# Performance work log

Hardware: AMD Instinct MI355X
Metric: run time of the kernel (lower is better)

Reference implementation:

```python
import jax, jax.numpy as jnp
import numpy as np

EMB = 256
HID = 512
VOCAB = 32000
SRC_LEN = 50
TRG_LEN = 50
BATCH = 64


def lstm_layer(x, h0, c0, Wih, Whh, b):
    """x: [T,B,in]; h0,c0: [B,H]; Wih: [4H,in]; Whh: [4H,H]; b: [4H].
    PyTorch gate order i,f,g,o. Returns (ys [T,B,H], hT, cT)."""
    def step(carry, xt):
        h, c = carry
        g = xt @ Wih.T + h @ Whh.T + b
        i, f, gg, o = jnp.split(g, 4, axis=-1)
        c = jax.nn.sigmoid(f) * c + jax.nn.sigmoid(i) * jnp.tanh(gg)
        h = jax.nn.sigmoid(o) * jnp.tanh(c)
        return (h, c), h
    (hT, cT), ys = jax.lax.scan(step, (h0, c0), x)
    return ys, hT, cT


def setup_inputs() -> dict:
    key = jax.random.key(0)
    ks = jax.random.split(key, 20)
    s = 0.05
    d = {
        'src': jax.random.randint(ks[0], (SRC_LEN, BATCH), 0, VOCAB),
        'trg': jax.random.randint(ks[1], (TRG_LEN, BATCH), 0, VOCAB),
        'enc_emb': jax.random.normal(ks[2], (VOCAB, EMB), jnp.float32) * s,
        'enc_Wih0': jax.random.normal(ks[3], (4 * HID, EMB), jnp.float32) * s,
        'enc_Whh0': jax.random.normal(ks[4], (4 * HID, HID), jnp.float32) * s,
        'enc_b0': jnp.zeros((4 * HID,), jnp.float32),
        'enc_Wih1': jax.random.normal(ks[5], (4 * HID, HID), jnp.float32) * s,
        'enc_Whh1': jax.random.normal(ks[6], (4 * HID, HID), jnp.float32) * s,
        'enc_b1': jnp.zeros((4 * HID,), jnp.float32),
        'dec_emb': jax.random.normal(ks[7], (VOCAB, EMB), jnp.float32) * s,
        'dec_Wih0': jax.random.normal(ks[8], (4 * HID, EMB), jnp.float32) * s,
        'dec_Whh0': jax.random.normal(ks[9], (4 * HID, HID), jnp.float32) * s,
        'dec_b0': jnp.zeros((4 * HID,), jnp.float32),
        'dec_Wih1': jax.random.normal(ks[10], (4 * HID, HID), jnp.float32) * s,
        'dec_Whh1': jax.random.normal(ks[11], (4 * HID, HID), jnp.float32) * s,
        'dec_b1': jnp.zeros((4 * HID,), jnp.float32),
        'out_W': jax.random.normal(ks[12], (VOCAB, HID), jnp.float32) * s,
        'out_b': jnp.zeros((VOCAB,), jnp.float32),
    }
    return d


def reference(src, trg, enc_emb, enc_Wih0, enc_Whh0, enc_b0, enc_Wih1, enc_Whh1,
              enc_b1, dec_emb, dec_Wih0, dec_Whh0, dec_b0, dec_Wih1, dec_Whh1,
              dec_b1, out_W, out_b):
    B = src.shape[1]
    z = jnp.zeros((B, HID), enc_emb.dtype)
    # Encoder: 2-layer LSTM over src, keep final (h, c) per layer
    xe = enc_emb[src]                                   # [S,B,E]
    y0, h0, c0 = lstm_layer(xe, z, z, enc_Wih0, enc_Whh0, enc_b0)
    _, h1, c1 = lstm_layer(y0, z, z, enc_Wih1, enc_Whh1, enc_b1)
    # Decoder with teacher forcing: inputs are trg[0:T-1]
    xd = dec_emb[trg[:-1]]                              # [T-1,B,E]
    d0, _, _ = lstm_layer(xd, h0, c0, dec_Wih0, dec_Whh0, dec_b0)
    d1, _, _ = lstm_layer(d0, h1, c1, dec_Wih1, dec_Whh1, dec_b1)
    preds = d1 @ out_W.T + out_b                        # [T-1,B,V]
    return preds
```

## Files before the change

kernel.cpp:

```cpp
#include <hip/hip_runtime.h>
#include <hip/hip_bf16.h>

#define BATCH 64
#define HID 512
#define EMB 256
#define VOCAB 32000
#define G4 2048

typedef __attribute__((ext_vector_type(8))) short short8;
typedef __attribute__((ext_vector_type(4))) float f32x4;
typedef __attribute__((ext_vector_type(4))) unsigned short ush4;

__global__ __launch_bounds__(256) void zero_kernel(float* p, int n){
    int i = blockIdx.x*256 + threadIdx.x;
    if (i < n) p[i] = 0.f;
}

__device__ __forceinline__ unsigned short bf16_rne(float x){
    unsigned b = __float_as_uint(x);
    return (unsigned short)((b + 0x7fffu + ((b >> 16) & 1u)) >> 16);
}
__device__ __forceinline__ void split2(float x, unsigned short& h, unsigned short& l){
    h = bf16_rne(x);
    l = bf16_rne(x - __uint_as_float((unsigned)h << 16));
}

__global__ __launch_bounds__(256) void embed_kernel(const int* __restrict__ tok,
                                                    const float* __restrict__ emb,
                                                    float* __restrict__ out, int T){
    int i = blockIdx.x*256 + threadIdx.x;
    int n = T*BATCH*(EMB/4);
    if (i >= n) return;
    int e4 = i % (EMB/4);
    int tb = i / (EMB/4);
    int id = tok[tb];
    reinterpret_cast<float4*>(out)[(size_t)tb*(EMB/4) + e4] =
        reinterpret_cast<const float4*>(emb + (size_t)id*EMB)[e4];
}

__global__ __launch_bounds__(256) void embed_plane_kernel(const int* __restrict__ tok,
                                                          const float* __restrict__ emb,
                                                          unsigned short* __restrict__ hi,
                                                          unsigned short* __restrict__ lo, int T){
    int i = blockIdx.x*256 + threadIdx.x;
    int n = T*BATCH*(EMB/4);
    if (i >= n) return;
    int e4 = i % (EMB/4);
    int tb = i / (EMB/4);
    int id = tok[tb];
    f32x4 v = reinterpret_cast<const f32x4*>(emb + (size_t)id*EMB)[e4];
    ush4 h, l;
    #pragma unroll
    for (int j = 0; j < 4; j++){ unsigned short a,b; split2(v[j], a, b); h[j]=a; l[j]=b; }
    reinterpret_cast<ush4*>(hi)[(size_t)tb*(EMB/4) + e4] = h;
    reinterpret_cast<ush4*>(lo)[(size_t)tb*(EMB/4) + e4] = l;
}

__global__ __launch_bounds__(256) void split_kernel(const float* __restrict__ in,
                                                    unsigned short* __restrict__ hi,
                                                    unsigned short* __restrict__ lo, int n4){
    int i = blockIdx.x*256 + threadIdx.x;
    if (i >= n4) return;
    f32x4 v = reinterpret_cast<const f32x4*>(in)[i];
    ush4 h, l;
    #pragma unroll
    for (int j = 0; j < 4; j++){ unsigned short a,b; split2(v[j], a, b); h[j]=a; l[j]=b; }
    reinterpret_cast<ush4*>(hi)[i] = h;
    reinterpret_cast<ush4*>(lo)[i] = l;
}

__global__ __launch_bounds__(256) void split_hi_kernel(const float* __restrict__ in,
                                                       unsigned short* __restrict__ hi, int n4){
    int i = blockIdx.x*256 + threadIdx.x;
    if (i >= n4) return;
    f32x4 v = reinterpret_cast<const f32x4*>(in)[i];
    ush4 h;
    #pragma unroll
    for (int j = 0; j < 4; j++) h[j] = bf16_rne(v[j]);
    reinterpret_cast<ush4*>(hi)[i] = h;
}

template<int KDIM, int NDIM>
__global__ __launch_bounds__(256) void gemm_mfma_split(
    const float* __restrict__ A, const float* __restrict__ B,
    const float* __restrict__ bias, float* __restrict__ C, int M)
{
    constexpr int LS = 40;
    __shared__ unsigned short Ah[128*LS], Al[128*LS], Bh[128*LS], Bl[128*LS];
    const int n0 = blockIdx.x*128, m0 = blockIdx.y*128;
    const int tid  = threadIdx.x;
    const int lane = tid & 63, wid = tid >> 6;
    const int wm = wid >> 1, wn = wid & 1;
    const int srow = tid >> 1, sk = (tid & 1)*16;
    f32x4 acc[4][4] = {};

    for (int k0 = 0; k0 < KDIM; k0 += 32){
        __syncthreads();
        {
            int ar = m0 + srow;
            float xv[16];
            if (ar < M){
                const float4* ap = reinterpret_cast<const float4*>(A + (size_t)ar*KDIM + k0 + sk);
                #pragma unroll
                for (int q = 0; q < 4; q++){
                    float4 v = ap[q];
                    xv[q*4+0]=v.x; xv[q*4+1]=v.y; xv[q*4+2]=v.z; xv[q*4+3]=v.w;
                }
            } else {
                #pragma unroll
                for (int q = 0; q < 16; q++) xv[q] = 0.f;
            }
            #pragma unroll
            for (int q = 0; q < 16; q++){
                unsigned short h,l; split2(xv[q], h, l);
                Ah[srow*LS + sk + q] = h;
                Al[srow*LS + sk + q] = l;
            }
        }
        {
            int br = n0 + srow;
            const float4* bp = reinterpret_cast<const float4*>(B + (size_t)br*KDIM + k0 + sk);
            #pragma unroll
            for (int q = 0; q < 4; q++){
                float4 v = bp[q];
                float xs[4] = {v.x, v.y, v.z, v.w};
                #pragma unroll
                for (int j = 0; j < 4; j++){
                    unsigned short h,l; split2(xs[j], h, l);
                    Bh[srow*LS + sk + q*4 + j] = h;
                    Bl[srow*LS + sk + q*4 + j] = l;
                }
            }
        }
        __syncthreads();
        const int fr = lane & 15, fk = (lane >> 4)*8;
        short8 a_h[4], a_l[4], b_h[4], b_l[4];
        #pragma unroll
        for (int mi = 0; mi < 4; mi++){
            int row = wm*64 + mi*16 + fr;
            a_h[mi] = *reinterpret_cast<const short8*>(&Ah[row*LS + fk]);
            a_l[mi] = *reinterpret_cast<const short8*>(&Al[row*LS + fk]);
        }
        #pragma unroll
        for (int nj = 0; nj < 4; nj++){
            int rowb = wn*64 + nj*16 + fr;
            b_h[nj] = *reinterpret_cast<const short8*>(&Bh[rowb*LS + fk]);
            b_l[nj] = *reinterpret_cast<const short8*>(&Bl[rowb*LS + fk]);
        }
        #pragma unroll
        for (int mi = 0; mi < 4; mi++)
            #pragma unroll
            for (int nj = 0; nj < 4; nj++){
                acc[mi][nj] = __builtin_amdgcn_mfma_f32_16x16x32_bf16(a_h[mi], b_h[nj], acc[mi][nj], 0,0,0);
                acc[mi][nj] = __builtin_amdgcn_mfma_f32_16x16x32_bf16(a_h[mi], b_l[nj], acc[mi][nj], 0,0,0);
                acc[mi][nj] = __builtin_amdgcn_mfma_f32_16x16x32_bf16(a_l[mi], b_h[nj], acc[mi][nj], 0,0,0);
            }
    }
    const int fr = lane & 15, fq = lane >> 4;
    #pragma unroll
    for (int nj = 0; nj < 4; nj++){
        int col = n0 + wn*64 + nj*16 + fr;
        float bv = bias[col];
        #pragma unroll
        for (int mi = 0; mi < 4; mi++){
            int rbase = m0 + wm*64 + mi*16 + fq*4;
            #pragma unroll
            for (int j = 0; j < 4; j++){
                int row = rbase + j;
                if (row < M)
                    __builtin_nontemporal_store(acc[mi][nj][j] + bv, &C[(size_t)row*NDIM + col]);
            }
        }
    }
}

__device__ __forceinline__ void gll16(const unsigned short* g, unsigned short* l){
    __builtin_amdgcn_global_load_lds(
        (const __attribute__((address_space(1))) unsigned int*)g,
        (__attribute__((address_space(3))) unsigned int*)l, 16, 0, 0);
}

template<int KDIM, int NDIM, int NTN>
__global__ __launch_bounds__(256) void gemm_planes_gll(
    const unsigned short* __restrict__ Ahi, const unsigned short* __restrict__ Alo,
    const unsigned short* __restrict__ Bhi, const unsigned short* __restrict__ Blo,
    const float* __restrict__ bias, float* __restrict__ C, int M)
{
    __shared__ unsigned short P[4][128*32];
    const int total = gridDim.x;
    const int q = total >> 3, r8 = total & 7;
    const int xcd = blockIdx.x & 7, idx = blockIdx.x >> 3;
    const int lid = (xcd < r8 ? xcd*(q+1) : r8*(q+1) + (xcd - r8)*q) + idx;
    const int m0 = (lid / NTN)*128, n0 = (lid % NTN)*128;

    const int tid  = threadIdx.x;
    const int lane = tid & 63, wid = tid >> 6;
    const int wm = wid >> 1, wn = wid & 1;

    const unsigned short* gsrc = (wid == 0) ? Ahi : (wid == 1) ? Alo
                               : (wid == 2) ? Bhi : Blo;
    const int row0 = (wid < 2) ? m0 : n0;
    const unsigned short* gbase = gsrc + (size_t)(row0 + (lane >> 2))*KDIM
                                       + 8*((lane & 3) ^ ((lane >> 3) & 3));
    unsigned short* lbase = &P[wid][0];

    f32x4 acc[4][4] = {};

    for (int k0 = 0; k0 < KDIM; k0 += 32){
        __syncthreads();
        #pragma unroll
        for (int i = 0; i < 8; i++)
            gll16(gbase + k0 + (size_t)i*16*KDIM, lbase + i*512);
        __syncthreads();

        const int fr = lane & 15, fkq = lane >> 4;
        const int swz = 8*(fkq ^ ((fr >> 1) & 3));
        short8 a_h[4], a_l[4], b_h[4], b_l[4];
        #pragma unroll
        for (int mi = 0; mi < 4; mi++){
            int row = wm*64 + mi*16 + fr;
            a_h[mi] = *reinterpret_cast<const short8*>(&P[0][row*32 + swz]);
            a_l[mi] = *reinterpret_cast<const short8*>(&P[1][row*32 + swz]);
        }
        #pragma unroll
        for (int nj = 0; nj < 4; nj++){
            int row = wn*64 + nj*16 + fr;
            b_h[nj] = *reinterpret_cast<const short8*>(&P[2][row*32 + swz]);
            b_l[nj] = *reinterpret_cast<const short8*>(&P[3][row*32 + swz]);
        }
        #pragma unroll
        for (int mi = 0; mi < 4; mi++)
            #pragma unroll
            for (int nj = 0; nj < 4; nj++){
                acc[mi][nj] = __builtin_amdgcn_mfma_f32_16x16x32_bf16(a_h[mi], b_h[nj], acc[mi][nj], 0,0,0);
                acc[mi][nj] = __builtin_amdgcn_mfma_f32_16x16x32_bf16(a_l[mi], b_h[nj], acc[mi][nj], 0,0,0);
                acc[mi][nj] = __builtin_amdgcn_mfma_f32_16x16x32_bf16(a_h[mi], b_l[nj], acc[mi][nj], 0,0,0);
            }
    }
    const int fr = lane & 15, fq = lane >> 4;
    #pragma unroll
    for (int nj = 0; nj < 4; nj++){
        int col = n0 + wn*64 + nj*16 + fr;
        float bv = bias[col];
        #pragma unroll
        for (int mi = 0; mi < 4; mi++){
            int rbase = m0 + wm*64 + mi*16 + fq*4;
            #pragma unroll
            for (int j = 0; j < 4; j++){
                int row = rbase + j;
                if (row < M)
                    __builtin_nontemporal_store(acc[mi][nj][j] + bv, &C[(size_t)row*NDIM + col]);
            }
        }
    }
}

template<int KDIM, int NDIM, int NTN>
__global__ __launch_bounds__(512) void gemm_planes_256w8(
    const unsigned short* __restrict__ Ahi,
    const unsigned short* __restrict__ Bhi,
    const float* __restrict__ bias, float* __restrict__ C, int M)
{
    __shared__ unsigned short Ah[256*32];
    __shared__ unsigned short Bh[128*32];
    const int total = gridDim.x;
    const int q = total >> 3, r8 = total & 7;
    const int xcd = blockIdx.x & 7, idx = blockIdx.x >> 3;
    const int lid = (xcd < r8 ? xcd*(q+1) : r8*(q+1) + (xcd - r8)*q) + idx;
    const int m0 = (lid / NTN)*256, n0 = (lid % NTN)*128;

    const int tid  = threadIdx.x;
    const int lane = tid & 63, wid = tid >> 6;
    const int wm = wid >> 1, wn = wid & 1;

    const bool stager = (wid < 6);
    const unsigned short* gsrc = (wid < 4) ? Ahi : Bhi;
    const int grow0 = (wid < 4) ? (m0 + wid*64) : (n0 + (wid - 4)*64);
    const unsigned short* gbase = gsrc + (size_t)(grow0 + (lane >> 2))*KDIM
                                       + 8*((lane & 3) ^ ((lane >> 3) & 3));
    unsigned short* lbase = (wid < 4) ? (Ah + wid*64*32) : (Bh + (wid - 4)*64*32);

    f32x4 acc[4][4] = {};

    for (int k0 = 0; k0 < KDIM; k0 += 32){
        __syncthreads();
        if (stager){
            #pragma unroll
            for (int i = 0; i < 4; i++)
                gll16(gbase + k0 + (size_t)i*16*KDIM, lbase + i*512);
        }
        __syncthreads();

        const int fr = lane & 15, fkq = lane >> 4;
        const int swz = 8*(fkq ^ ((fr >> 1) & 3));
        short8 a_h[4], b_h[4];
        #pragma unroll
        for (int nj = 0; nj < 4; nj++){
            int row = wn*64 + nj*16 + fr;
            b_h[nj] = *reinterpret_cast<const short8*>(&Bh[row*32 + swz]);
        }
        #pragma unroll
        for (int mi = 0; mi < 4; mi++){
            int row = wm*64 + mi*16 + fr;
            a_h[mi] = *reinterpret_cast<const short8*>(&Ah[row*32 + swz]);
        }
        #pragma unroll
        for (int mi = 0; mi < 4; mi++)
            #pragma unroll
            for (int nj = 0; nj < 4; nj++)
                acc[mi][nj] = __builtin_amdgcn_mfma_f32_16x16x32_bf16(a_h[mi], b_h[nj], acc[mi][nj], 0,0,0);
    }
    const int fr = lane & 15, fq = lane >> 4;
    #pragma unroll
    for (int nj = 0; nj < 4; nj++){
        int col = n0 + wn*64 + nj*16 + fr;
        float bv = bias[col];
        #pragma unroll
        for (int mi = 0; mi < 4; mi++){
            int rbase = m0 + wm*64 + mi*16 + fq*4;
            #pragma unroll
            for (int j = 0; j < 4; j++){
                int row = rbase + j;
                if (row < M)
                    __builtin_nontemporal_store(acc[mi][nj][j] + bv, &C[(size_t)row*NDIM + col]);
            }
        }
    }
}

__device__ __forceinline__ void lstm_body(
    const float* __restrict__ Xp, const float* __restrict__ Whh,
    const float* __restrict__ hinit, const float* __restrict__ cinit,
    float* __restrict__ ys, float* __restrict__ cfin,
    int T, unsigned* __restrict__ flagbase, int bx,
    unsigned short* __restrict__ phi, unsigned short* __restrict__ plo)
{
    constexpr int WS = 520;
    __shared__ unsigned short hH[8*WS], hL[8*WS];
    __shared__ __align__(16) float red[4*544 + 128];
    __shared__ unsigned short zbuf[8];

    const int hc  = bx & 31, bc = bx >> 5;
    const int hid0 = hc*16;
    const int tid = threadIdx.x;
    const int lane = tid & 63, kc = tid >> 6;
    const int fr = lane & 15, fkq = lane >> 4;
    unsigned* myflag = flagbase + (size_t)(bc*32 + hc)*16;

    if (tid < 8) zbuf[tid] = 0;

    short8 ah[4][4], al[4][4];
    #pragma unroll
    for (int m = 0; m < 4; m++){
        const float* wr = Whh + (size_t)(m*HID + hid0 + fr)*HID;
        #pragma unroll
        for (int s = 0; s < 4; s++){
            int k0 = kc*128 + s*32 + fkq*8;
            f32x4 v0 = *reinterpret_cast<const f32x4*>(wr + k0);
            f32x4 v1 = *reinterpret_cast<const f32x4*>(wr + k0 + 4);
            short8 h8, l8;
            float xv[8] = {v0[0],v0[1],v0[2],v0[3],v1[0],v1[1],v1[2],v1[3]};
            #pragma unroll
            for (int j = 0; j < 8; j++){
                unsigned short hh, ll; split2(xv[j], hh, ll);
                h8[j] = (short)hh; l8[j] = (short)ll;
            }
            ah[m][s] = h8; al[m][s] = l8;
        }
    }

    const int ub = tid >> 4;
    const int uh = tid & 15;
    float creg = 0.f;
    if (tid < 128) creg = cinit[(size_t)(bc*8 + ub)*HID + hid0 + uh];

    const size_t hbase = (size_t)bc*8*HID;
    const float* xprow = Xp + (size_t)(bc*8 + ub)*G4 + hid0 + uh;

    float xn0=0.f, xn1=0.f, xn2=0.f, xn3=0.f;
    if (tid < 128){
        const float* xpr = xprow;
        xn0 = xpr[0]; xn1 = xpr[512]; xn2 = xpr[1024]; xn3 = xpr[1536];
    }

    for (int t = 0; t < T; t++){
        {
            const f32x4* hsrc = reinterpret_cast<const f32x4*>(
                (t == 0) ? (hinit + hbase) : (ys + (size_t)(t-1)*BATCH*HID + hbase));
            #pragma unroll
            for (int j = 0; j < 4; j++){
                int fidx = tid + j*256;
                f32x4 v = hsrc[fidx];
                int e   = fidx*4;
                int row = e >> 9, col = e & 511;
                ush4 h, l;
                #pragma unroll
                for (int qq = 0; qq < 4; qq++){ unsigned short a,b; split2(v[qq], a, b); h[qq]=a; l[qq]=b; }
                *reinterpret_cast<ush4*>(&hH[row*WS + col]) = h;
                *reinterpret_cast<ush4*>(&hL[row*WS + col]) = l;
            }
        }
        __syncthreads();

        {
            f32x4 acc4[4] = {};
            const bool breal = fr < 8;
            #pragma unroll
            for (int s = 0; s < 4; s++){
                int k0 = kc*128 + s*32 + fkq*8;
                short8 bh = breal ? *reinterpret_cast<const short8*>(&hH[fr*WS + k0])
                                  : *reinterpret_cast<const short8*>(zbuf);
                short8 bl = breal ? *reinterpret_cast<const short8*>(&hL[fr*WS + k0])
                                  : *reinterpret_cast<const short8*>(zbuf);
                #pragma unroll
                for (int m = 0; m < 4; m++){
                    acc4[m] = __builtin_amdgcn_mfma_f32_16x16x32_bf16(ah[m][s], bh, acc4[m], 0,0,0);
                    acc4[m] = __builtin_amdgcn_mfma_f32_16x16x32_bf16(ah[m][s], bl, acc4[m], 0,0,0);
                    acc4[m] = __builtin_amdgcn_mfma_f32_16x16x32_bf16(al[m][s], bh, acc4[m], 0,0,0);
                }
            }
            const int b = lane & 15;
            if (b < 8){
                #pragma unroll
                for (int m = 0; m < 4; m++)
                    *reinterpret_cast<f32x4*>(&red[kc*544 + b*68 + m*16 + (lane >> 4)*4]) = acc4[m];
            }
        }
        __syncthreads();

        if (tid < 64){
            #pragma unroll
            for (int b = 0; b < 8; b++)
                red[b*68 + tid] = red[b*68 + tid] + red[544 + b*68 + tid]
                               + red[1088 + b*68 + tid] + red[1632 + b*68 + tid];
        }
        __syncthreads();

        if (tid < 128){
            float gi = red[ub*68 + 0*16 + uh] + xn0;
            float gf = red[ub*68 + 1*16 + uh] + xn1;
            float gg = red[ub*68 + 2*16 + uh] + xn2;
            float go = red[ub*68 + 3*16 + uh] + xn3;
            float si = 1.f/(1.f + expf(-gi));
            float sf = 1.f/(1.f + expf(-gf));
            float so = 1.f/(1.f + expf(-go));
            float tg = tanhf(gg);
            float c = sf*creg + si*tg;
            creg = c;
            float hval = so * tanhf(c);
            red[2176 + tid] = hval;
            if (phi){
                unsigned short hh, ll; split2(hval, hh, ll);
                size_t poff = (size_t)t*BATCH*HID + (size_t)(bc*8 + ub)*HID + hid0 + uh;
                phi[poff] = hh; plo[poff] = ll;
            }
            if (t < T-1){
                const float* xpr = xprow + (size_t)(t+1)*BATCH*G4;
                xn0 = xpr[0]; xn1 = xpr[512]; xn2 = xpr[1024]; xn3 = xpr[1536];
            }
        }
        __syncthreads();

        if (tid < 64){
            if (tid < 32){
                f32x4 v = *reinterpret_cast<const f32x4*>(&red[2176 + tid*4]);
                const f32x4* addr = reinterpret_cast<const f32x4*>(
                    ys + (size_t)t*BATCH*HID
                       + (size_t)(bc*8 + (tid >> 2))*HID + hid0 + (tid & 3)*4);
                asm volatile("global_store_dwordx4 %0, %1, off sc0 sc1"
                             :: "v"(addr), "v"(v) : "memory");
            }
            if (t < T-1){
                asm volatile("s_waitcnt vmcnt(0)" ::: "memory");
                if (tid == 0)
                    __hip_atomic_store(myflag, (unsigned)(t+1),
                                       __ATOMIC_RELAXED, __HIP_MEMORY_SCOPE_AGENT);
                const unsigned tgt = (unsigned)(t+1);
                unsigned* fp = flagbase + (size_t)(bc*32 + (tid & 31))*16;
                unsigned spins = 0;
                bool done = false;
                while (!done && spins < (1u<<20)){
                    unsigned v = tgt;
                    if (tid < 32)
                        v = __hip_atomic_load(fp, __ATOMIC_RELAXED, __HIP_MEMORY_SCOPE_AGENT);
                    done = (bool)__all((int)(v >= tgt));
                    spins++;
                }
            }
        }
        __syncthreads();
    }

    if (tid < 128)
        cfin[(size_t)(bc*8 + ub)*HID + hid0 + uh] = creg;
}

__global__ __launch_bounds__(256, 2) void lstm_layer_k(
    const float* Xp, const float* Whh, const float* hinit, const float* cinit,
    float* ys, float* cfin, int T, unsigned* flagbase,
    unsigned short* phi, unsigned short* plo)
{
    lstm_body(Xp, Whh, hinit, cinit, ys, cfin, T, flagbase, blockIdx.x, phi, plo);
}

__global__ __launch_bounds__(256, 2) void lstm_dual_k(
    const float* Xp0, const float* Whh0, const float* hi0, const float* ci0,
    float* ys0, float* cf0, int T0, unsigned* fl0,
    unsigned short* phi0, unsigned short* plo0,
    const float* Xp1, const float* Whh1, const float* hi1, const float* ci1,
    float* ys1, float* cf1, int T1, unsigned* fl1,
    unsigned short* phi1, unsigned short* plo1)
{
    const int role = blockIdx.x >> 8;
    const int bx = blockIdx.x & 255;
    if (role == 0)
        lstm_body(Xp0, Whh0, hi0, ci0, ys0, cf0, T0, fl0, bx, phi0, plo0);
    else
        lstm_body(Xp1, Whh1, hi1, ci1, ys1, cf1, T1, fl1, bx, phi1, plo1);
}

extern "C" void kernel_launch(void* const* d_in, const int* in_sizes, int n_in,
                              void* d_out, int out_size, void* d_ws, size_t ws_size,
                              hipStream_t stream) {
    const int*   src      = (const int*)  d_in[0];
    const int*   trg      = (const int*)  d_in[1];
    const float* enc_emb  = (const float*)d_in[2];
    const float* enc_Wih0 = (const float*)d_in[3];
    const float* enc_Whh0 = (const float*)d_in[4];
    const float* enc_b0   = (const float*)d_in[5];
    const float* enc_Wih1 = (const float*)d_in[6];
    const float* enc_Whh1 = (const float*)d_in[7];
    const float* enc_b1   = (const float*)d_in[8];
    const float* dec_emb  = (const float*)d_in[9];
    const float* dec_Wih0 = (const float*)d_in[10];
    const float* dec_Whh0 = (const float*)d_in[11];
    const float* dec_b0   = (const float*)d_in[12];
    const float* dec_Wih1 = (const float*)d_in[13];
    const float* dec_Whh1 = (const float*)d_in[14];
    const float* dec_b1   = (const float*)d_in[15];
    const float* out_W    = (const float*)d_in[16];
    const float* out_b    = (const float*)d_in[17];

    float* ob = (float*)d_out;
    float* Xp   = ob;
    float* xe   = ob + (size_t)6553600;
    float* xd   = ob + (size_t)7372800;
    float* eys0 = ob + (size_t)8175616;
    float* eys1 = ob + (size_t)9814016;
    float* dys0 = ob + (size_t)11452416;
    float* Xp2  = ob + (size_t)13058048;

    float* ws = (float*)d_ws;
    float* dys1 = ws;
    float* c0   = ws + (size_t)1605632;
    float* c1   = ws + (size_t)1638400;
    float* hz   = ws + (size_t)1671168;
    unsigned* flags = (unsigned*)(ws + (size_t)1703936);
    unsigned short* Whi = (unsigned short*)(ws + (size_t)1720320);
    unsigned short* Wlo = Whi + (size_t)16384000;
    unsigned short* Ahi = Wlo + (size_t)16384000;
    unsigned short* Alo = Ahi + (size_t)1703936;
    unsigned short* eW0h = Alo  + (size_t)1703936;
    unsigned short* eW0l = eW0h + (size_t)524288;
    unsigned short* eW1h = eW0l + (size_t)524288;
    unsigned short* eW1l = eW1h + (size_t)1048576;
    unsigned short* dW0h = eW1l + (size_t)1048576;
    unsigned short* dW0l = dW0h + (size_t)524288;
    unsigned short* dW1h = dW0l + (size_t)524288;
    unsigned short* dW1l = dW1h + (size_t)1048576;
    unsigned short* XAh  = dW1l + (size_t)1048576;
    unsigned short* XAl  = XAh  + (size_t)1638400;
    const size_t end_xp = (size_t)1720320*4 +
        2*((size_t)16384000*2 + (size_t)1703936*2 + (size_t)524288*4 +
           (size_t)1048576*4 + (size_t)1638400*2);
    const bool xp_ok = (ws_size >= end_xp);

    {
        int n = 3*BATCH*HID + 4*4096;
        zero_kernel<<<(n+255)/256, 256, 0, stream>>>(c0, n);
    }

    if (xp_ok){
        split_hi_kernel<<<(16384000/4 + 255)/256, 256, 0, stream>>>(out_W, Whi, 16384000/4);
        split_kernel<<<(524288/4 + 255)/256, 256, 0, stream>>>(enc_Wih0, eW0h, eW0l, 524288/4);
        split_kernel<<<(1048576/4 + 255)/256, 256, 0, stream>>>(enc_Wih1, eW1h, eW1l, 1048576/4);
        split_kernel<<<(524288/4 + 255)/256, 256, 0, stream>>>(dec_Wih0, dW0h, dW0l, 524288/4);
        split_kernel<<<(1048576/4 + 255)/256, 256, 0, stream>>>(dec_Wih1, dW1h, dW1l, 1048576/4);
        embed_plane_kernel<<<(50*BATCH*(EMB/4)+255)/256, 256, 0, stream>>>(src, enc_emb, XAh, XAl, 50);
        embed_plane_kernel<<<(49*BATCH*(EMB/4)+255)/256, 256, 0, stream>>>(trg, dec_emb, Ahi, Alo, 49);
    } else {
        embed_kernel<<<(50*BATCH*(EMB/4)+255)/256, 256, 0, stream>>>(src, enc_emb, xe, 50);
        embed_kernel<<<(49*BATCH*(EMB/4)+255)/256, 256, 0, stream>>>(trg, dec_emb, xd, 49);
    }

    dim3 xgrid(G4/128, 25);

    if (xp_ok)
        gemm_planes_gll<EMB, G4, 16><<<400, 256, 0, stream>>>(XAh, XAl, eW0h, eW0l, enc_b0, Xp, 3200);
    else
        gemm_mfma_split<EMB, G4><<<xgrid, 256, 0, stream>>>(xe, enc_Wih0, enc_b0, Xp, 3200);
    lstm_layer_k<<<256, 256, 0, stream>>>(Xp, enc_Whh0, hz, hz, eys0, c0, 50, flags + 0,
                                          xp_ok ? XAh : nullptr, XAl);

    if (xp_ok){
        gemm_planes_gll<HID, G4, 16><<<400, 256, 0, stream>>>(XAh, XAl, eW1h, eW1l, enc_b1, Xp, 3200);
        gemm_planes_gll<EMB, G4, 16><<<400, 256, 0, stream>>>(Ahi, Alo, dW0h, dW0l, dec_b0, Xp2, 3136);
    } else {
        gemm_mfma_split<HID, G4><<<xgrid, 256, 0, stream>>>(eys0, enc_Wih1, enc_b1, Xp, 3200);
        gemm_mfma_split<EMB, G4><<<xgrid, 256, 0, stream>>>(xd, dec_Wih0, dec_b0, Xp2, 3136);
    }

    lstm_dual_k<<<512, 256, 0, stream>>>(
        Xp,  enc_Whh1, hz,                          hz, eys1, c1, 50, flags + 4096,  nullptr, nullptr,
        Xp2, dec_Whh0, eys0 + (size_t)49*BATCH*HID, c0, dys0, c0, 49, flags + 8192,
        xp_ok ? XAh : nullptr, XAl);

    if (xp_ok)
        gemm_planes_gll<HID, G4, 16><<<400, 256, 0, stream>>>(XAh, XAl, dW1h, dW1l, dec_b1, Xp, 3136);
    else
        gemm_mfma_split<HID, G4><<<xgrid, 256, 0, stream>>>(dys0, dec_Wih1, dec_b1, Xp, 3136);
    lstm_layer_k<<<256, 256, 0, stream>>>(Xp, dec_Whh1, eys1 + (size_t)49*BATCH*HID, c1,
                                          dys1, c1, 49, flags + 12288,
                                          xp_ok ? Ahi : nullptr, Alo);

    if (xp_ok){
        gemm_planes_256w8<HID, VOCAB, 250><<<13*250, 512, 0, stream>>>(
            Ahi, Whi, out_b, (float*)d_out, 3136);
    } else {
        gemm_mfma_split<HID, VOCAB><<<dim3(VOCAB/128, 25), 256, 0, stream>>>(
            dys1, out_W, out_b, (float*)d_out, 3136);
    }
}
```

Baseline: 957.1 us.

## Overlap decoder input GEMM with encoder LSTM and fuse weight-split launches

Merges the five weight-splitting kernels into one launch to save launch overhead. Adds a combined kernel whose first 256 blocks run the encoder layer-0 LSTM recurrence while the remaining 400 blocks compute the decoder layer-0 input projection GEMM, so the GEMM fills CUs the latency-bound LSTM leaves idle. It also changes the LSTM block-to-(batch chunk, hidden chunk) mapping so batch chunks interleave across XCDs. The risk is that the persistent, flag-synchronised LSTM blocks could be delayed or starved if GEMM blocks occupy resources, and the remap changes cache locality.

```diff
diff --git a/kernel.cpp b/kernel.cpp
--- a/kernel.cpp
+++ b/kernel.cpp
@@ -69,15 +69,35 @@
     reinterpret_cast<ush4*>(lo)[i] = l;
 }
 
-__global__ __launch_bounds__(256) void split_hi_kernel(const float* __restrict__ in,
-                                                       unsigned short* __restrict__ hi, int n4){
+__global__ __launch_bounds__(256) void split_all_kernel(
+    const float* __restrict__ outW, unsigned short* __restrict__ Whi,
+    const float* __restrict__ w0, unsigned short* __restrict__ w0h, unsigned short* __restrict__ w0l,
+    const float* __restrict__ w1, unsigned short* __restrict__ w1h, unsigned short* __restrict__ w1l,
+    const float* __restrict__ w2, unsigned short* __restrict__ w2h, unsigned short* __restrict__ w2l,
+    const float* __restrict__ w3, unsigned short* __restrict__ w3h, unsigned short* __restrict__ w3l)
+{
     int i = blockIdx.x*256 + threadIdx.x;
-    if (i >= n4) return;
-    f32x4 v = reinterpret_cast<const f32x4*>(in)[i];
-    ush4 h;
+    if (i < 4096000){
+        f32x4 v = reinterpret_cast<const f32x4*>(outW)[i];
+        ush4 h;
+        #pragma unroll
+        for (int j = 0; j < 4; j++) h[j] = bf16_rne(v[j]);
+        reinterpret_cast<ush4*>(Whi)[i] = h;
+        return;
+    }
+    i -= 4096000;
+    const float* src; unsigned short* dh; unsigned short* dl;
+    if (i < 131072){ src = w0; dh = w0h; dl = w0l; }
+    else if (i < 131072+262144){ i -= 131072; src = w1; dh = w1h; dl = w1l; }
+    else if (i < 131072+262144+131072){ i -= 131072+262144; src = w2; dh = w2h; dl = w2l; }
+    else if (i < 131072+262144+131072+262144){ i -= 131072+262144+131072; src = w3; dh = w3h; dl = w3l; }
+    else return;
+    f32x4 v = reinterpret_cast<const f32x4*>(src)[i];
+    ush4 h, l;
     #pragma unroll
-    for (int j = 0; j < 4; j++) h[j] = bf16_rne(v[j]);
-    reinterpret_cast<ush4*>(hi)[i] = h;
+    for (int j = 0; j < 4; j++){ unsigned short a,b; split2(v[j], a, b); h[j]=a; l[j]=b; }
+    reinterpret_cast<ush4*>(dh)[i] = h;
+    reinterpret_cast<ush4*>(dl)[i] = l;
 }
 
 template<int KDIM, int NDIM>
@@ -181,15 +201,15 @@
 }
 
 template<int KDIM, int NDIM, int NTN>
-__global__ __launch_bounds__(256) void gemm_planes_gll(
+__device__ __forceinline__ void gemm_gll_body(
     const unsigned short* __restrict__ Ahi, const unsigned short* __restrict__ Alo,
     const unsigned short* __restrict__ Bhi, const unsigned short* __restrict__ Blo,
-    const float* __restrict__ bias, float* __restrict__ C, int M)
+    const float* __restrict__ bias, float* __restrict__ C, int M,
+    int bid_raw, int total)
 {
     __shared__ unsigned short P[4][128*32];
-    const int total = gridDim.x;
     const int q = total >> 3, r8 = total & 7;
-    const int xcd = blockIdx.x & 7, idx = blockIdx.x >> 3;
+    const int xcd = bid_raw & 7, idx = bid_raw >> 3;
     const int lid = (xcd < r8 ? xcd*(q+1) : r8*(q+1) + (xcd - r8)*q) + idx;
     const int m0 = (lid / NTN)*128, n0 = (lid % NTN)*128;
 
@@ -253,6 +273,16 @@
             }
         }
     }
+}
+
+template<int KDIM, int NDIM, int NTN>
+__global__ __launch_bounds__(256) void gemm_planes_gll(
+    const unsigned short* Ahi, const unsigned short* Alo,
+    const unsigned short* Bhi, const unsigned short* Blo,
+    const float* bias, float* C, int M)
+{
+    gemm_gll_body<KDIM, NDIM, NTN>(Ahi, Alo, Bhi, Blo, bias, C, M,
+                                   blockIdx.x, gridDim.x);
 }
 
 template<int KDIM, int NDIM, int NTN>
@@ -340,7 +370,7 @@
     __shared__ __align__(16) float red[4*544 + 128];
     __shared__ unsigned short zbuf[8];
 
-    const int hc  = bx & 31, bc = bx >> 5;
+    const int bc  = bx & 7, hc = bx >> 3;
     const int hid0 = hc*16;
     const int tid = threadIdx.x;
     const int lane = tid & 63, kc = tid >> 6;
@@ -517,6 +547,21 @@
         lstm_body(Xp0, Whh0, hi0, ci0, ys0, cf0, T0, fl0, bx, phi0, plo0);
     else
         lstm_body(Xp1, Whh1, hi1, ci1, ys1, cf1, T1, fl1, bx, phi1, plo1);
+}
+
+__global__ __launch_bounds__(256, 2) void lstm_gemm_k(
+    const float* Xp, const float* Whh, const float* hinit, const float* cinit,
+    float* ys, float* cfin, int T, unsigned* flagbase,
+    unsigned short* phi, unsigned short* plo,
+    const unsigned short* gAhi, const unsigned short* gAlo,
+    const unsigned short* gBhi, const unsigned short* gBlo,
+    const float* gbias, float* gC, int gM, int gTotal)
+{
+    if ((int)blockIdx.x < 256)
+        lstm_body(Xp, Whh, hinit, cinit, ys, cfin, T, flagbase, blockIdx.x, phi, plo);
+    else
+        gemm_gll_body<EMB, G4, 16>(gAhi, gAlo, gBhi, gBlo, gbias, gC, gM,
+                                   blockIdx.x - 256, gTotal);
 }
 
 extern "C" void kernel_launch(void* const* d_in, const int* in_sizes, int n_in,
@@ -581,11 +626,10 @@
     }
 
     if (xp_ok){
-        split_hi_kernel<<<(16384000/4 + 255)/256, 256, 0, stream>>>(out_W, Whi, 16384000/4);
-        split_kernel<<<(524288/4 + 255)/256, 256, 0, stream>>>(enc_Wih0, eW0h, eW0l, 524288/4);
-        split_kernel<<<(1048576/4 + 255)/256, 256, 0, stream>>>(enc_Wih1, eW1h, eW1l, 1048576/4);
-        split_kernel<<<(524288/4 + 255)/256, 256, 0, stream>>>(dec_Wih0, dW0h, dW0l, 524288/4);
-        split_kernel<<<(1048576/4 + 255)/256, 256, 0, stream>>>(dec_Wih1, dW1h, dW1l, 1048576/4);
+        split_all_kernel<<<(4882432 + 255)/256, 256, 0, stream>>>(
+            out_W, Whi,
+            enc_Wih0, eW0h, eW0l,  enc_Wih1, eW1h, eW1l,
+            dec_Wih0, dW0h, dW0l,  dec_Wih1, dW1h, dW1l);
         embed_plane_kernel<<<(50*BATCH*(EMB/4)+255)/256, 256, 0, stream>>>(src, enc_emb, XAh, XAl, 50);
         embed_plane_kernel<<<(49*BATCH*(EMB/4)+255)/256, 256, 0, stream>>>(trg, dec_emb, Ahi, Alo, 49);
     } else {
@@ -599,16 +643,21 @@
         gemm_planes_gll<EMB, G4, 16><<<400, 256, 0, stream>>>(XAh, XAl, eW0h, eW0l, enc_b0, Xp, 3200);
     else
         gemm_mfma_split<EMB, G4><<<xgrid, 256, 0, stream>>>(xe, enc_Wih0, enc_b0, Xp, 3200);
-    lstm_layer_k<<<256, 256, 0, stream>>>(Xp, enc_Whh0, hz, hz, eys0, c0, 50, flags + 0,
-                                          xp_ok ? XAh : nullptr, XAl);
 
     if (xp_ok){
+        lstm_gemm_k<<<656, 256, 0, stream>>>(
+            Xp, enc_Whh0, hz, hz, eys0, c0, 50, flags + 0, XAh, XAl,
+            Ahi, Alo, dW0h, dW0l, dec_b0, Xp2, 3136, 400);
+    } else {
+        lstm_layer_k<<<256, 256, 0, stream>>>(Xp, enc_Whh0, hz, hz, eys0, c0, 50, flags + 0,
+                                              nullptr, nullptr);
+        gemm_mfma_split<EMB, G4><<<xgrid, 256, 0, stream>>>(xd, dec_Wih0, dec_b0, Xp2, 3136);
+    }
+
+    if (xp_ok)
         gemm_planes_gll<HID, G4, 16><<<400, 256, 0, stream>>>(XAh, XAl, eW1h, eW1l, enc_b1, Xp, 3200);
-        gemm_planes_gll<EMB, G4, 16><<<400, 256, 0, stream>>>(Ahi, Alo, dW0h, dW0l, dec_b0, Xp2, 3136);
-    } else {
+    else
         gemm_mfma_split<HID, G4><<<xgrid, 256, 0, stream>>>(eys0, enc_Wih1, enc_b1, Xp, 3200);
-        gemm_mfma_split<EMB, G4><<<xgrid, 256, 0, stream>>>(xd, dec_Wih0, dec_b0, Xp2, 3136);
-    }
 
     lstm_dual_k<<<512, 256, 0, stream>>>(
         Xp,  enc_Whh1, hz,                          hz, eys1, c1, 50, flags + 4096,  nullptr, nullptr,
```

Result: no change. 945.8 us (-1.2%).
